# Kernel tuning notes

Hardware: AMD Instinct MI355X
Metric: run time of the kernel (lower is better)

The kernel has to match this reference:

```python
import jax, jax.numpy as jnp
import numpy as np

IN_C, OUT_C, K, STRIDE, PAD = 128, 256, 3, 1, 1


def setup_inputs() -> dict:
    key = jax.random.key(0)
    kx, kw = jax.random.split(key)
    x = jax.random.normal(kx, (32, IN_C, 56, 56), dtype=jnp.float32)
    weight = jax.random.normal(kw, (OUT_C, IN_C, K, K), dtype=jnp.float32) * 0.02
    bias = jnp.zeros((OUT_C,), dtype=jnp.float32)
    return {"x": x, "weight": weight, "bias": bias}


def reference(x, weight, bias):
    # Faithful conv2d: zero-pad + im2col + GEMM in the torch module is
    # mathematically a standard cross-correlation conv; use the fused primitive.
    out = jax.lax.conv_general_dilated(
        x, weight,
        window_strides=(STRIDE, STRIDE),
        padding=[(PAD, PAD), (PAD, PAD)],
        dimension_numbers=("NCHW", "OIHW", "NCHW"),
    )
    out = out + bias[None, :, None, None]
    return out
```

## Files before the change

### kernel.cpp

```cpp
#include <hip/hip_runtime.h>


typedef __attribute__((ext_vector_type(8))) short short8;
typedef __attribute__((ext_vector_type(4))) float f32x4;
typedef unsigned short ushort_t;

#define HWSZ 56
#define HW2 3136
#define INC 128
#define OUTC 256
#define PADW 58
#define XT_ELEMS 13778944

__device__ __forceinline__ ushort_t f2b(float f) {
    union { float f; unsigned u; } v; v.f = f;
    unsigned r = v.u + 0x7fffu + ((v.u >> 16) & 1u);
    return (ushort_t)(r >> 16);
}

__device__ __forceinline__ void glds16(const void* g, void* l) {
    __builtin_amdgcn_global_load_lds(
        (const __attribute__((address_space(1))) unsigned*)g,
        (__attribute__((address_space(3))) unsigned*)l, 16, 0, 0);
}

__global__ __launch_bounds__(256) void halo_zero(ushort_t* __restrict__ xt) {
    const int tid = blockIdx.x * 256 + threadIdx.x;
    const int g = tid & 15;
    const int p = tid >> 4;
    const int n = p / 228;
    const int bp = p - n * 228;
    int h, wv;
    if (bp < 58)       { h = 0;        wv = bp; }
    else if (bp < 116) { h = 57;       wv = bp - 58; }
    else if (bp < 172) { h = bp - 115; wv = 0; }
    else               { h = bp - 171; wv = 57; }
    const short8 z = {0,0,0,0,0,0,0,0};
    *reinterpret_cast<short8*>(xt + (((size_t)n * PADW + h) * PADW + wv) * INC + g * 8) = z;
}

__global__ __launch_bounds__(256) void xt_kernel(const float* __restrict__ x,
                                                 ushort_t* __restrict__ xt) {
    __shared__ float tile[128][65];
    const int b = blockIdx.x;
    const int n = b / 49;
    const int hw0 = (b - n * 49) * 64;
    const int t = threadIdx.x;

    const float* xp = x + (size_t)n * (INC * HW2) + hw0;
    const int c_base = t >> 4;
    const int hwo = (t & 15) * 4;
#pragma unroll
    for (int j = 0; j < 8; ++j) {
        const int c = j * 16 + c_base;
        const f32x4 v = *reinterpret_cast<const f32x4*>(xp + c * HW2 + hwo);
        tile[c][hwo + 0] = v[0];
        tile[c][hwo + 1] = v[1];
        tile[c][hwo + 2] = v[2];
        tile[c][hwo + 3] = v[3];
    }
    __syncthreads();
    const int hw = t >> 2;
    const int q = t & 3;
    const int P = hw0 + hw;
    const int oh = P / HWSZ;
    const int ow = P - oh * HWSZ;
    ushort_t* dst = xt + (((size_t)n * PADW + oh + 1) * PADW + (ow + 1)) * INC;
#pragma unroll
    for (int g = 0; g < 4; ++g) {
        short8 v;
#pragma unroll
        for (int e = 0; e < 8; ++e) v[e] = (short)f2b(tile[g * 32 + q * 8 + e][hw]);
        *reinterpret_cast<short8*>(dst + g * 32 + q * 8) = v;
    }
}

__global__ __launch_bounds__(256) void wt_kernel(const float* __restrict__ w,
                                                 ushort_t* __restrict__ wt2) {
    const int tid = blockIdx.x * 256 + threadIdx.x;
    const int panel = tid >> 9;
    const int s = tid & 511;
    const int oc_tile = panel / 36;
    const int rem = panel - oc_tile * 36;
    const int pos = rem >> 2;
    const int icc = rem & 3;
    const int row = s >> 2;
    const int fq = (s & 3) ^ ((row >> 1) & 3);
    const int oc = oc_tile * 128 + row;
    const int ic0 = icc * 32 + fq * 8;
    short8 v;
#pragma unroll
    for (int e = 0; e < 8; ++e) v[e] = (short)f2b(w[(oc * 128 + ic0 + e) * 9 + pos]);
    *reinterpret_cast<short8*>(wt2 + (size_t)tid * 8) = v;
}

__global__ __launch_bounds__(256, 3) void conv_main(const ushort_t* __restrict__ xt,
                                                    const ushort_t* __restrict__ wt2,
                                                    const float* __restrict__ bias,
                                                    float* __restrict__ out) {
    __shared__ ushort_t lds[3][2][4096];

    const int bid = blockIdx.x;
    const int work = (bid & 7) * 196 + (bid >> 3);
    const int oc_tile = work & 1;
    const int P0 = (work >> 1) * 128;

    const int t = threadIdx.x;
    const int w = t >> 6;
    const int l = t & 63;
    const int fr = l & 15;
    const int fq = l >> 4;
    const int wr = w >> 1;
    const int wc = w & 1;

    const ushort_t* Abase = wt2 + (size_t)oc_tile * (36 * 4096) + t * 8;

    const int pa = w * 16 + (l >> 2);
    const int Pa = P0 + pa;
    const int na = Pa / HW2; const int hwa = Pa - na * HW2;
    const int oha = hwa / HWSZ; const int owa = hwa - oha * HWSZ;
    const int Pb = Pa + 64;
    const int nb = Pb / HW2; const int hwb = Pb - nb * HW2;
    const int ohb = hwb / HWSZ; const int owb = hwb - ohb * HWSZ;
    const ushort_t* xra = xt + (((size_t)na * PADW + oha) * PADW + owa) * INC;
    const ushort_t* xrb = xt + (((size_t)nb * PADW + ohb) * PADW + owb) * INC;
    const int swz = ((l & 3) ^ ((l >> 3) & 3)) * 8;

    const int frag_off = fr * 32 + ((fq ^ ((fr >> 1) & 3)) * 8);

    f32x4 acc[4][4];
#pragma unroll
    for (int i = 0; i < 4; ++i)
#pragma unroll
        for (int j = 0; j < 4; ++j) { f32x4 z = {0.f,0.f,0.f,0.f}; acc[i][j] = z; }

    auto stage = [&](int s1, int bsel) {
        const int pos = s1 >> 2;
        const int icc = s1 & 3;
        const int kh = pos / 3;
        const int kw = pos - kh * 3;
        const int koff = (kh * PADW + kw) * INC + icc * 32;
        const ushort_t* Ab = Abase + s1 * 4096;
        glds16(Ab,               &lds[bsel][0][w * 512]);
        glds16(Ab + 2048,        &lds[bsel][0][(w + 4) * 512]);
        glds16(xra + koff + swz, &lds[bsel][1][w * 512]);
        glds16(xrb + koff + swz, &lds[bsel][1][(w + 4) * 512]);
    };

    auto compute = [&](int bsel) {
        const ushort_t* A = &lds[bsel][0][0];
        const ushort_t* B = &lds[bsel][1][0];
        short8 af[4], bf[4];
#pragma unroll
        for (int mi = 0; mi < 4; ++mi)
            af[mi] = *reinterpret_cast<const short8*>(A + wr * 2048 + mi * 512 + frag_off);
#pragma unroll
        for (int ni = 0; ni < 4; ++ni)
            bf[ni] = *reinterpret_cast<const short8*>(B + wc * 2048 + ni * 512 + frag_off);
        __builtin_amdgcn_s_setprio(1);
#pragma unroll
        for (int mi = 0; mi < 4; ++mi)
#pragma unroll
            for (int ni = 0; ni < 4; ++ni)
                acc[mi][ni] = __builtin_amdgcn_mfma_f32_16x16x32_bf16(af[mi], bf[ni],
                                                                      acc[mi][ni], 0, 0, 0);
        __builtin_amdgcn_s_setprio(0);
    };

    stage(0, 0);
    stage(1, 1);

    int bc = 0, bn = 2;
    for (int s = 0; s < 35; ++s) {
        asm volatile("s_waitcnt vmcnt(4)\n\ts_barrier" ::: "memory");
        if (s < 34) stage(s + 2, bn);
        compute(bc);
        bc = (bc == 2) ? 0 : bc + 1;
        bn = (bn == 2) ? 0 : bn + 1;
    }
    asm volatile("s_waitcnt vmcnt(0)\n\ts_barrier" ::: "memory");
    compute(bc);

    const int oc0 = oc_tile * 128;
    float bmr[4][4];
#pragma unroll
    for (int mi = 0; mi < 4; ++mi)
#pragma unroll
        for (int r = 0; r < 4; ++r)
            bmr[mi][r] = bias[oc0 + wr * 64 + mi * 16 + fq * 4 + r];

#pragma unroll
    for (int ni = 0; ni < 4; ++ni) {
        const int Pp = P0 + wc * 64 + ni * 16 + fr;
        const int nn = Pp / HW2;
        const int hwp = Pp - nn * HW2;
        float* op = out + (size_t)nn * (OUTC * HW2) + hwp;
#pragma unroll
        for (int mi = 0; mi < 4; ++mi)
#pragma unroll
            for (int r = 0; r < 4; ++r) {
                const int oc = oc0 + wr * 64 + mi * 16 + fq * 4 + r;
                op[oc * HW2] = acc[mi][ni][r] + bmr[mi][r];
            }
    }
}

extern "C" void kernel_launch(void* const* d_in, const int* in_sizes, int n_in,
                              void* d_out, int out_size, void* d_ws, size_t ws_size,
                              hipStream_t stream) {
    const float* x = (const float*)d_in[0];
    const float* w = (const float*)d_in[1];
    const float* bias = (const float*)d_in[2];
    float* out = (float*)d_out;

    ushort_t* xt = (ushort_t*)d_ws;
    ushort_t* wt2 = xt + XT_ELEMS;

    halo_zero<<<456, 256, 0, stream>>>(xt);
    xt_kernel<<<1568, 256, 0, stream>>>(x, xt);
    wt_kernel<<<144, 256, 0, stream>>>(w, wt2);
    conv_main<<<1568, 256, 0, stream>>>(xt, wt2, bias, out);
}
```

Measured before the change: 203.4 us.

## Double conv tile along the pixel dimension to 128x256 per block

New measurement: 205.5 us. Within noise of the previous version (+1.0%).

```diff
diff --git a/kernel.cpp b/kernel.cpp
--- a/kernel.cpp
+++ b/kernel.cpp
@@ -94,16 +94,16 @@
     *reinterpret_cast<short8*>(wt2 + (size_t)tid * 8) = v;
 }
 
-__global__ __launch_bounds__(256, 3) void conv_main(const ushort_t* __restrict__ xt,
+__global__ __launch_bounds__(256, 2) void conv_main(const ushort_t* __restrict__ xt,
                                                     const ushort_t* __restrict__ wt2,
                                                     const float* __restrict__ bias,
                                                     float* __restrict__ out) {
-    __shared__ ushort_t lds[3][2][4096];
+    __shared__ ushort_t lds[3][12288];
 
     const int bid = blockIdx.x;
-    const int work = (bid & 7) * 196 + (bid >> 3);
+    const int work = (bid & 7) * 98 + (bid >> 3);
     const int oc_tile = work & 1;
-    const int P0 = (work >> 1) * 128;
+    const int P0 = (work >> 1) * 256;
 
     const int t = threadIdx.x;
     const int w = t >> 6;
@@ -115,24 +115,31 @@
 
     const ushort_t* Abase = wt2 + (size_t)oc_tile * (36 * 4096) + t * 8;
 
-    const int pa = w * 16 + (l >> 2);
-    const int Pa = P0 + pa;
-    const int na = Pa / HW2; const int hwa = Pa - na * HW2;
-    const int oha = hwa / HWSZ; const int owa = hwa - oha * HWSZ;
-    const int Pb = Pa + 64;
-    const int nb = Pb / HW2; const int hwb = Pb - nb * HW2;
-    const int ohb = hwb / HWSZ; const int owb = hwb - ohb * HWSZ;
-    const ushort_t* xra = xt + (((size_t)na * PADW + oha) * PADW + owa) * INC;
-    const ushort_t* xrb = xt + (((size_t)nb * PADW + ohb) * PADW + owb) * INC;
     const int swz = ((l & 3) ^ ((l >> 3) & 3)) * 8;
+    const ushort_t* xr0;
+    const ushort_t* xr1;
+    const ushort_t* xr2;
+    const ushort_t* xr3;
+    {
+        const ushort_t* tmp[4];
+#pragma unroll
+        for (int k = 0; k < 4; ++k) {
+            const int row = (w + 4 * k) * 16 + (l >> 2);
+            const int P = P0 + row;
+            const int n = P / HW2; const int hw = P - n * HW2;
+            const int oh = hw / HWSZ; const int ow = hw - oh * HWSZ;
+            tmp[k] = xt + (((size_t)n * PADW + oh) * PADW + ow) * INC + swz;
+        }
+        xr0 = tmp[0]; xr1 = tmp[1]; xr2 = tmp[2]; xr3 = tmp[3];
+    }
 
     const int frag_off = fr * 32 + ((fq ^ ((fr >> 1) & 3)) * 8);
 
-    f32x4 acc[4][4];
+    f32x4 acc[4][8];
 #pragma unroll
     for (int i = 0; i < 4; ++i)
 #pragma unroll
-        for (int j = 0; j < 4; ++j) { f32x4 z = {0.f,0.f,0.f,0.f}; acc[i][j] = z; }
+        for (int j = 0; j < 8; ++j) { f32x4 z = {0.f,0.f,0.f,0.f}; acc[i][j] = z; }
 
     auto stage = [&](int s1, int bsel) {
         const int pos = s1 >> 2;
@@ -141,22 +148,24 @@
         const int kw = pos - kh * 3;
         const int koff = (kh * PADW + kw) * INC + icc * 32;
         const ushort_t* Ab = Abase + s1 * 4096;
-        glds16(Ab,               &lds[bsel][0][w * 512]);
-        glds16(Ab + 2048,        &lds[bsel][0][(w + 4) * 512]);
-        glds16(xra + koff + swz, &lds[bsel][1][w * 512]);
-        glds16(xrb + koff + swz, &lds[bsel][1][(w + 4) * 512]);
+        glds16(Ab,          &lds[bsel][w * 512]);
+        glds16(Ab + 2048,   &lds[bsel][(w + 4) * 512]);
+        glds16(xr0 + koff,  &lds[bsel][4096 + (w +  0) * 512]);
+        glds16(xr1 + koff,  &lds[bsel][4096 + (w +  4) * 512]);
+        glds16(xr2 + koff,  &lds[bsel][4096 + (w +  8) * 512]);
+        glds16(xr3 + koff,  &lds[bsel][4096 + (w + 12) * 512]);
     };
 
     auto compute = [&](int bsel) {
-        const ushort_t* A = &lds[bsel][0][0];
-        const ushort_t* B = &lds[bsel][1][0];
+        const ushort_t* A = &lds[bsel][0];
+        const ushort_t* B = &lds[bsel][4096];
         short8 af[4], bf[4];
 #pragma unroll
         for (int mi = 0; mi < 4; ++mi)
             af[mi] = *reinterpret_cast<const short8*>(A + wr * 2048 + mi * 512 + frag_off);
 #pragma unroll
         for (int ni = 0; ni < 4; ++ni)
-            bf[ni] = *reinterpret_cast<const short8*>(B + wc * 2048 + ni * 512 + frag_off);
+            bf[ni] = *reinterpret_cast<const short8*>(B + wc * 4096 + ni * 512 + frag_off);
         __builtin_amdgcn_s_setprio(1);
 #pragma unroll
         for (int mi = 0; mi < 4; ++mi)
@@ -165,6 +174,17 @@
                 acc[mi][ni] = __builtin_amdgcn_mfma_f32_16x16x32_bf16(af[mi], bf[ni],
                                                                       acc[mi][ni], 0, 0, 0);
         __builtin_amdgcn_s_setprio(0);
+#pragma unroll
+        for (int ni = 0; ni < 4; ++ni)
+            bf[ni] = *reinterpret_cast<const short8*>(B + wc * 4096 + (ni + 4) * 512 + frag_off);
+        __builtin_amdgcn_s_setprio(1);
+#pragma unroll
+        for (int mi = 0; mi < 4; ++mi)
+#pragma unroll
+            for (int ni = 0; ni < 4; ++ni)
+                acc[mi][ni + 4] = __builtin_amdgcn_mfma_f32_16x16x32_bf16(af[mi], bf[ni],
+                                                                          acc[mi][ni + 4], 0, 0, 0);
+        __builtin_amdgcn_s_setprio(0);
     };
 
     stage(0, 0);
@@ -172,7 +192,7 @@
 
     int bc = 0, bn = 2;
     for (int s = 0; s < 35; ++s) {
-        asm volatile("s_waitcnt vmcnt(4)\n\ts_barrier" ::: "memory");
+        asm volatile("s_waitcnt vmcnt(6)\n\ts_barrier" ::: "memory");
         if (s < 34) stage(s + 2, bn);
         compute(bc);
         bc = (bc == 2) ? 0 : bc + 1;
@@ -190,8 +210,8 @@
             bmr[mi][r] = bias[oc0 + wr * 64 + mi * 16 + fq * 4 + r];
 
 #pragma unroll
-    for (int ni = 0; ni < 4; ++ni) {
-        const int Pp = P0 + wc * 64 + ni * 16 + fr;
+    for (int ni = 0; ni < 8; ++ni) {
+        const int Pp = P0 + wc * 128 + ni * 16 + fr;
         const int nn = Pp / HW2;
         const int hwp = Pp - nn * HW2;
         float* op = out + (size_t)nn * (OUTC * HW2) + hwp;
@@ -219,5 +239,5 @@
     halo_zero<<<456, 256, 0, stream>>>(xt);
     xt_kernel<<<1568, 256, 0, stream>>>(x, xt);
     wt_kernel<<<144, 256, 0, stream>>>(w, wt2);
-    conv_main<<<1568, 256, 0, stream>>>(xt, wt2, bias, out);
-}
+    conv_main<<<784, 256, 0, stream>>>(xt, wt2, bias, out);
+}
```
